# Performance work log

Hardware: AMD Instinct MI355X
Metric: run time of the kernel (lower is better)

Reference implementation:

```python
import jax, jax.numpy as jnp
import numpy as np

D_MODEL = 1024
N_HEAD = 16
HEAD_DIM = D_MODEL // N_HEAD


def setup_inputs() -> dict:
    key = jax.random.key(0)
    ks = jax.random.split(key, 8)
    B, T, C = 4, 2048, D_MODEL
    scale = 1.0 / np.sqrt(C)
    return {
        "q": jax.random.normal(ks[0], (B, T, C), dtype=jnp.float32),
        "k": jax.random.normal(ks[1], (B, T, C), dtype=jnp.float32),
        "v": jax.random.normal(ks[2], (B, T, C), dtype=jnp.float32),
        # torch.nn.Linear weights are (out_features, in_features)
        "Wq": jax.random.normal(ks[3], (C, C), dtype=jnp.float32) * scale,
        "Wk": jax.random.normal(ks[4], (C, C), dtype=jnp.float32) * scale,
        "Wv": jax.random.normal(ks[5], (C, C), dtype=jnp.float32) * scale,
        "Wo": jax.random.normal(ks[6], (C, C), dtype=jnp.float32) * scale,
        "bo": jax.random.normal(ks[7], (C,), dtype=jnp.float32) * scale,
    }


def reference(q, k, v, Wq, Wk, Wv, Wo, bo):
    B, T, C = q.shape
    # projections (torch Linear: x @ W.T), split into heads -> (B, H, T, Dh)
    def split_heads(x, W):
        y = jnp.einsum('btc,oc->bto', x, W)
        return y.reshape(B, T, N_HEAD, HEAD_DIM).transpose(0, 2, 1, 3)

    qh = split_heads(q, Wq)
    kh = split_heads(k, Wk)
    vh = split_heads(v, Wv)

    # scaled dot-product attention with full T x T scores (as in source)
    scores = jnp.einsum('bhqd,bhkd->bhqk', qh, kh) / jnp.sqrt(
        jnp.asarray(HEAD_DIM, dtype=qh.dtype))
    attn = jax.nn.softmax(scores, axis=-1)
    out = jnp.einsum('bhqk,bhkd->bhqd', attn, vh)

    out = out.transpose(0, 2, 1, 3).reshape(B, T, C)
    # output projection (with bias); dropout is identity in eval mode
    return jnp.einsum('btc,oc->bto', out, Wo) + bo
```

## Files before the change

kernel.cpp:

```cpp
#include <hip/hip_runtime.h>

#define TSEQ  2048
#define NB    4
#define CDIM  1024
#define NHEAD 16
#define DH    64
#define MROWS (NB*TSEQ)

using bf16x8 = __attribute__((ext_vector_type(8))) __bf16;
using f32x4  = __attribute__((ext_vector_type(4))) float;
using u16x8  = __attribute__((ext_vector_type(8))) unsigned short;

__device__ __forceinline__ unsigned short f2bf(float x) {
  unsigned u = __float_as_uint(x);
  u += 0x7fffu + ((u >> 16) & 1u);
  return (unsigned short)(u >> 16);
}

__device__ __forceinline__ unsigned pkp(float lo, float hi) {
  return __builtin_amdgcn_perm(__float_as_uint(hi), __float_as_uint(lo), 0x07060302u);
}

__device__ __forceinline__ float fexp2(float x) {
  float r;
  asm("v_exp_f32 %0, %1" : "=v"(r) : "v"(x));
  return r;
}

__device__ __forceinline__ void gload_lds16(const void* g, void* l) {
  __builtin_amdgcn_global_load_lds(
      (const __attribute__((address_space(1))) void*)g,
      (__attribute__((address_space(3))) void*)l,
      16, 0, 0);
}

__global__ void cast3_f32_bf16(const float* __restrict__ a, const float* __restrict__ b,
                               const float* __restrict__ c, unsigned short* __restrict__ out,
                               int n) {
  const float* src = (blockIdx.y == 0) ? a : (blockIdx.y == 1) ? b : c;
  int i = (blockIdx.x * 256 + threadIdx.x) * 8;
  if (i >= n) return;
  float4 x = *(const float4*)(src + i);
  float4 y = *(const float4*)(src + i + 4);
  u16x8 r;
  r[0] = f2bf(x.x); r[1] = f2bf(x.y); r[2] = f2bf(x.z); r[3] = f2bf(x.w);
  r[4] = f2bf(y.x); r[5] = f2bf(y.y); r[6] = f2bf(y.z); r[7] = f2bf(y.w);
  *(u16x8*)(out + (size_t)blockIdx.y * n + i) = r;
}

__global__ void cast4_f32_bf16(const float* __restrict__ a, const float* __restrict__ b,
                               const float* __restrict__ c, const float* __restrict__ d,
                               unsigned short* __restrict__ out, int n) {
  const float* src = (blockIdx.y == 0) ? a : (blockIdx.y == 1) ? b
                   : (blockIdx.y == 2) ? c : d;
  int i = (blockIdx.x * 256 + threadIdx.x) * 8;
  if (i >= n) return;
  float4 x = *(const float4*)(src + i);
  float4 y = *(const float4*)(src + i + 4);
  u16x8 r;
  r[0] = f2bf(x.x); r[1] = f2bf(x.y); r[2] = f2bf(x.z); r[3] = f2bf(x.w);
  r[4] = f2bf(y.x); r[5] = f2bf(y.y); r[6] = f2bf(y.z); r[7] = f2bf(y.w);
  *(u16x8*)(out + (size_t)blockIdx.y * n + i) = r;
}

template<int MODE>
__global__ __launch_bounds__(256)
void gemm_bt(const unsigned short* __restrict__ A,
             const unsigned short* __restrict__ Bw,
             void* __restrict__ Cout,
             const float* __restrict__ bias,
             float qscale)
{
  constexpr int K  = CDIM;
  constexpr int BK = 64;
  __shared__ __attribute__((aligned(16))) unsigned short As[128 * BK];
  __shared__ __attribute__((aligned(16))) unsigned short Bs[128 * BK];

  const int tid = threadIdx.x;
  const int l   = tid & 63, w = tid >> 6;
  const int l16 = l & 15,  lq = l >> 4;
  const int wm  = w >> 1,  wn = w & 1;

  const int pz = (MODE == 0) ? blockIdx.z : 0;
  A  += (size_t)pz * MROWS * CDIM;
  Bw += (size_t)pz * CDIM * CDIM;
  const float oscale = (MODE == 0 && pz == 0) ? qscale : 1.0f;

  const int nwg  = gridDim.x * gridDim.y;
  const int orig = blockIdx.y * gridDim.x + blockIdx.x;
  const int wg   = (orig & 7) * (nwg >> 3) + (orig >> 3);
  const int m0   = (wg / gridDim.x) * 128, n0 = (wg % gridDim.x) * 128;

  f32x4 acc[4][4] = {};

  int srow[4], scol[4];
#pragma unroll
  for (int i = 0; i < 4; ++i) {
    int r = (i * 256 + tid) >> 3;
    srow[i] = r;
    scol[i] = (((tid & 7) ^ (r & 7)) << 3);
  }

  for (int kt = 0; kt < K; kt += BK) {
#pragma unroll
    for (int i = 0; i < 4; ++i) {
      gload_lds16(A  + (size_t)(m0 + srow[i]) * K + kt + scol[i],
                  (char*)As + (i * 256 + w * 64) * 16);
      gload_lds16(Bw + (size_t)(n0 + srow[i]) * K + kt + scol[i],
                  (char*)Bs + (i * 256 + w * 64) * 16);
    }
    __syncthreads();

#pragma unroll
    for (int kk = 0; kk < 2; ++kk) {
      bf16x8 af[4], bfr[4];
#pragma unroll
      for (int mi = 0; mi < 4; ++mi) {
        int row = wm * 64 + mi * 16 + l16;
        af[mi] = *(const bf16x8*)&As[row * BK + (((kk * 4 + lq) ^ (row & 7)) << 3)];
      }
#pragma unroll
      for (int nj = 0; nj < 4; ++nj) {
        int row = wn * 64 + nj * 16 + l16;
        bfr[nj] = *(const bf16x8*)&Bs[row * BK + (((kk * 4 + lq) ^ (row & 7)) << 3)];
      }
#pragma unroll
      for (int mi = 0; mi < 4; ++mi)
#pragma unroll
        for (int nj = 0; nj < 4; ++nj)
          acc[mi][nj] = __builtin_amdgcn_mfma_f32_16x16x32_bf16(af[mi], bfr[nj], acc[mi][nj], 0, 0, 0);
    }
    __syncthreads();
  }

#pragma unroll
  for (int mi = 0; mi < 4; ++mi) {
#pragma unroll
    for (int nj = 0; nj < 4; ++nj) {
      int gn = n0 + wn * 64 + nj * 16 + l16;
#pragma unroll
      for (int r = 0; r < 4; ++r) {
        int gm = m0 + wm * 64 + mi * 16 + lq * 4 + r;
        float v = acc[mi][nj][r];
        if constexpr (MODE == 0) {
          int b = gm >> 11, t = gm & (TSEQ - 1);
          int h = gn >> 6,  d = gn & 63;
          ((unsigned short*)Cout)[(size_t)pz * MROWS * CDIM +
              ((((size_t)b * NHEAD + h) * TSEQ + t) << 6) + d] = f2bf(v * oscale);
        } else {
          ((float*)Cout)[(size_t)gm * CDIM + gn] = v + bias[gn];
        }
      }
    }
  }
}

__global__ __launch_bounds__(256, 3)
void attn_fwd(const unsigned short* __restrict__ Qh,
              const unsigned short* __restrict__ Kh,
              const unsigned short* __restrict__ Vh,
              unsigned short* __restrict__ O)
{
  __shared__ __attribute__((aligned(16))) unsigned short Ks[2][64 * DH];
  __shared__ __attribute__((aligned(16))) unsigned short Vt[2][DH * 64];

  const int tid = threadIdx.x;
  const int l   = tid & 63, w = tid >> 6;
  const int l16 = l & 15,  lq = l >> 4;

  const int orig    = blockIdx.y * gridDim.x + blockIdx.x;
  const int logical = (orig & 7) * 128 + (orig >> 3);
  const int bh  = logical >> 4;
  const int q0  = (logical & 15) * 128;
  const size_t base = (size_t)bh * TSEQ * DH;

  bf16x8 qfA0, qfA1, qfB0, qfB1;
  {
    const unsigned short* qp = Qh + base + (size_t)(q0 + w * 32 + l16) * DH + lq * 8;
    qfA0 = *(const bf16x8*)qp;
    qfA1 = *(const bf16x8*)(qp + 32);
    qfB0 = *(const bf16x8*)(qp + 16 * DH);
    qfB1 = *(const bf16x8*)(qp + 16 * DH + 32);
  }

  union { unsigned short u[8]; bf16x8 v; } onesu;
#pragma unroll
  for (int i = 0; i < 8; ++i) onesu.u[i] = 0x3F80;
  const bf16x8 ones = onesu.v;

  f32x4 oaccA[4] = {}, oaccB[4] = {};
  f32x4 laccA = {}, laccB = {};

  const int vc  = tid & 7;
  const int vu  = tid >> 3;
  const int kva = ((vu >> 4) << 5) | (vu & 15);
  const int vslot = ((vu >> 4) << 5) | (((vu >> 2) & 3) << 3) |
                    ((vu & 1) << 2) | (((vu >> 1) & 1) << 1);

  int vAddr[8];
#pragma unroll
  for (int j = 0; j < 8; ++j) {
    int d = vc * 8 + j;
    vAddr[j] = ((d << 7) + (vslot << 1)) ^ ((((d & 7) ^ (d >> 3)) & 7) << 4);
  }
  int kAddr[8];
#pragma unroll
  for (int nj = 0; nj < 4; ++nj) {
    int row = nj * 16 + l16;
    kAddr[nj * 2 + 0] = (row << 7) + ((lq       ^ (row & 7)) << 4);
    kAddr[nj * 2 + 1] = (row << 7) + (((4 + lq) ^ (row & 7)) << 4);
  }
  int pvAddr[8];
#pragma unroll
  for (int dj = 0; dj < 4; ++dj) {
    int d  = dj * 16 + l16;
    int cx = (((d & 7) ^ (d >> 3)) & 7) << 4;
    pvAddr[dj * 2 + 0] = (((d << 6) + (lq << 3)) << 1) ^ cx;
    pvAddr[dj * 2 + 1] = (((d << 6) + 32 + (lq << 3)) << 1) ^ cx;
  }

  constexpr int TILE_STRIDE = 64 * DH;
  const int krow = tid >> 3;
  const int kcol = ((tid & 7) ^ (krow & 7)) << 3;
  const unsigned short* kPtr = Kh + base + (size_t)krow * DH + kcol;
  const unsigned short* vPtr = Vh + base + (size_t)kva * DH + vc * 8;

  auto stageK = [&](int bb) {
    gload_lds16(kPtr,           (char*)Ks + bb * 8192 + (w * 64) * 16);
    gload_lds16(kPtr + 32 * DH, (char*)Ks + bb * 8192 + (256 + w * 64) * 16);
  };
  auto loadV = [&](u16x8& v0, u16x8& v1) {
    v0 = *(const u16x8*)vPtr;
    v1 = *(const u16x8*)(vPtr + 16 * DH);
  };
  auto writeV = [&](int bb, u16x8 v0, u16x8 v1) {
    union { u16x8 v; unsigned u[4]; } a, b;
    a.v = v0; b.v = v1;
    char* vb = (char*)Vt + bb * 8192;
#pragma unroll
    for (int r = 0; r < 4; ++r) {
      unsigned w0 = __builtin_amdgcn_perm(b.u[r], a.u[r], 0x05040100u);
      unsigned w1 = __builtin_amdgcn_perm(b.u[r], a.u[r], 0x07060302u);
      *(unsigned*)(vb + vAddr[2 * r])     = w0;
      *(unsigned*)(vb + vAddr[2 * r + 1]) = w1;
    }
  };

  {
    u16x8 v0, v1;
    loadV(v0, v1);
    stageK(0);
    writeV(0, v0, v1);
    kPtr += TILE_STRIDE;
    vPtr += TILE_STRIDE;
  }
  __syncthreads();

  constexpr int NT = TSEQ / 64;

  auto body = [&](int bb, bool PF) {
    u16x8 nv0, nv1;
    if (PF) {
      loadV(nv0, nv1);
      stageK(bb ^ 1);
      kPtr += TILE_STRIDE;
      vPtr += TILE_STRIDE;
    }

    f32x4 sA[4] = {}, sB[4] = {};
    __builtin_amdgcn_s_setprio(1);
#pragma unroll
    for (int nj = 0; nj < 4; ++nj) {
      bf16x8 kf0 = *(const bf16x8*)((const char*)Ks + bb * 8192 + kAddr[nj * 2 + 0]);
      bf16x8 kf1 = *(const bf16x8*)((const char*)Ks + bb * 8192 + kAddr[nj * 2 + 1]);
      sA[nj] = __builtin_amdgcn_mfma_f32_16x16x32_bf16(kf0, qfA0, sA[nj], 0, 0, 0);
      sA[nj] = __builtin_amdgcn_mfma_f32_16x16x32_bf16(kf1, qfA1, sA[nj], 0, 0, 0);
      sB[nj] = __builtin_amdgcn_mfma_f32_16x16x32_bf16(kf0, qfB0, sB[nj], 0, 0, 0);
      sB[nj] = __builtin_amdgcn_mfma_f32_16x16x32_bf16(kf1, qfB1, sB[nj], 0, 0, 0);
    }
    __builtin_amdgcn_s_setprio(0);

#pragma unroll
    for (int nj = 0; nj < 4; ++nj)
#pragma unroll
      for (int r = 0; r < 4; ++r) {
        sA[nj][r] = fexp2(sA[nj][r]);
        sB[nj][r] = fexp2(sB[nj][r]);
      }

    union { unsigned d[4]; bf16x8 v; } pA0, pA1, pB0, pB1;
    pA0.d[0] = pkp(sA[0][0], sA[1][0]); pA0.d[1] = pkp(sA[0][2], sA[1][2]);
    pA0.d[2] = pkp(sA[0][1], sA[1][1]); pA0.d[3] = pkp(sA[0][3], sA[1][3]);
    pA1.d[0] = pkp(sA[2][0], sA[3][0]); pA1.d[1] = pkp(sA[2][2], sA[3][2]);
    pA1.d[2] = pkp(sA[2][1], sA[3][1]); pA1.d[3] = pkp(sA[2][3], sA[3][3]);
    pB0.d[0] = pkp(sB[0][0], sB[1][0]); pB0.d[1] = pkp(sB[0][2], sB[1][2]);
    pB0.d[2] = pkp(sB[0][1], sB[1][1]); pB0.d[3] = pkp(sB[0][3], sB[1][3]);
    pB1.d[0] = pkp(sB[2][0], sB[3][0]); pB1.d[1] = pkp(sB[2][2], sB[3][2]);
    pB1.d[2] = pkp(sB[2][1], sB[3][1]); pB1.d[3] = pkp(sB[2][3], sB[3][3]);

    __builtin_amdgcn_s_setprio(1);
    laccA = __builtin_amdgcn_mfma_f32_16x16x32_bf16(pA0.v, ones, laccA, 0, 0, 0);
    laccA = __builtin_amdgcn_mfma_f32_16x16x32_bf16(pA1.v, ones, laccA, 0, 0, 0);
    laccB = __builtin_amdgcn_mfma_f32_16x16x32_bf16(pB0.v, ones, laccB, 0, 0, 0);
    laccB = __builtin_amdgcn_mfma_f32_16x16x32_bf16(pB1.v, ones, laccB, 0, 0, 0);
    __builtin_amdgcn_s_setprio(0);

    if (PF) writeV(bb ^ 1, nv0, nv1);

    __builtin_amdgcn_s_setprio(1);
#pragma unroll
    for (int dj = 0; dj < 4; ++dj) {
#pragma unroll
      for (int c = 0; c < 2; ++c) {
        bf16x8 vf = *(const bf16x8*)((const char*)Vt + bb * 8192 + pvAddr[dj * 2 + c]);
        oaccA[dj] = __builtin_amdgcn_mfma_f32_16x16x32_bf16(c ? pA1.v : pA0.v, vf, oaccA[dj], 0, 0, 0);
        oaccB[dj] = __builtin_amdgcn_mfma_f32_16x16x32_bf16(c ? pB1.v : pB0.v, vf, oaccB[dj], 0, 0, 0);
      }
    }
    __builtin_amdgcn_s_setprio(0);
    __syncthreads();
  };

  for (int tt = 0; tt < NT - 2; tt += 2) {
    body(0, true);
    body(1, true);
  }
  body(0, true);
  body(1, false);

  const int b = bh >> 4, h = bh & (NHEAD - 1);
#pragma unroll
  for (int r = 0; r < 4; ++r) {
    float invA = 1.f / laccA[r];
    float invB = 1.f / laccB[r];
    size_t obA = ((size_t)b * TSEQ + (q0 + w * 32 + lq * 4 + r)) * CDIM + h * DH;
    size_t obB = obA + (size_t)16 * CDIM;
#pragma unroll
    for (int dj = 0; dj < 4; ++dj) {
      O[obA + dj * 16 + l16] = f2bf(oaccA[dj][r] * invA);
      O[obB + dj * 16 + l16] = f2bf(oaccB[dj][r] * invB);
    }
  }
}

extern "C" void kernel_launch(void* const* d_in, const int* in_sizes, int n_in,
                              void* d_out, int out_size, void* d_ws, size_t ws_size,
                              hipStream_t stream) {
  const float* q  = (const float*)d_in[0];
  const float* k  = (const float*)d_in[1];
  const float* v  = (const float*)d_in[2];
  const float* Wq = (const float*)d_in[3];
  const float* Wk = (const float*)d_in[4];
  const float* Wv = (const float*)d_in[5];
  const float* Wo = (const float*)d_in[6];
  const float* bo = (const float*)d_in[7];

  char* ws = (char*)d_ws;
  const size_t SZ_ACT = (size_t)MROWS * CDIM * 2;
  const size_t SZ_W   = (size_t)CDIM * CDIM * 2;
  unsigned short* qb  = (unsigned short*)(ws);
  unsigned short* wqb = (unsigned short*)(ws + 3 * SZ_ACT);
  unsigned short* wob = (unsigned short*)(ws + 3 * SZ_ACT + 3 * SZ_W);
  unsigned short* Qh  = (unsigned short*)(ws + 3 * SZ_ACT + 4 * SZ_W);
  unsigned short* Kh  = (unsigned short*)(ws + 4 * SZ_ACT + 4 * SZ_W);
  unsigned short* Vh  = (unsigned short*)(ws + 5 * SZ_ACT + 4 * SZ_W);
  unsigned short* AttO = qb;

  const int nAct = MROWS * CDIM;
  const int nW   = CDIM * CDIM;

  cast3_f32_bf16<<<dim3(nAct / 2048, 3), 256, 0, stream>>>(q, k, v, qb, nAct);
  cast4_f32_bf16<<<dim3(nW / 2048, 4), 256, 0, stream>>>(Wq, Wk, Wv, Wo, wqb, nW);

  const float QSCALE = 0.18033688011112042f;

  gemm_bt<0><<<dim3(CDIM / 128, MROWS / 128, 3), 256, 0, stream>>>(
      qb, wqb, Qh, nullptr, QSCALE);

  attn_fwd<<<dim3(TSEQ / 128, NB * NHEAD), 256, 0, stream>>>(Qh, Kh, Vh, AttO);

  gemm_bt<1><<<dim3(CDIM / 128, MROWS / 128, 1), 256, 0, stream>>>(
      AttO, wob, (float*)d_out, bo, 1.0f);
}
```

Before: 192.6 us.

## Software-pipeline attention: overlap PV of previous tile with QK of current tile

Restructures the attention inner loop so each iteration computes QK^T and softmax exp for tile i while running the P·V MFMAs for tile i-1 in the same high-priority block. This needs a triple-buffered V tile in LDS and ping-pong P registers, with a prologue and epilogue for the first and last tiles. LDS address arrays are replaced by computed offsets to save registers. The aim is to hide exp/pack latency behind matrix work, at the cost of extra LDS and live registers, which may reduce occupancy.

```diff
diff --git a/kernel.cpp b/kernel.cpp
--- a/kernel.cpp
+++ b/kernel.cpp
@@ -33,6 +33,8 @@
       (__attribute__((address_space(3))) void*)l,
       16, 0, 0);
 }
+
+#define MFMA16(a, b, c) __builtin_amdgcn_mfma_f32_16x16x32_bf16((a), (b), (c), 0, 0, 0)
 
 __global__ void cast3_f32_bf16(const float* __restrict__ a, const float* __restrict__ b,
                                const float* __restrict__ c, unsigned short* __restrict__ out,
@@ -128,7 +130,7 @@
       for (int mi = 0; mi < 4; ++mi)
 #pragma unroll
         for (int nj = 0; nj < 4; ++nj)
-          acc[mi][nj] = __builtin_amdgcn_mfma_f32_16x16x32_bf16(af[mi], bfr[nj], acc[mi][nj], 0, 0, 0);
+          acc[mi][nj] = MFMA16(af[mi], bfr[nj], acc[mi][nj]);
     }
     __syncthreads();
   }
@@ -162,7 +164,7 @@
               unsigned short* __restrict__ O)
 {
   __shared__ __attribute__((aligned(16))) unsigned short Ks[2][64 * DH];
-  __shared__ __attribute__((aligned(16))) unsigned short Vt[2][DH * 64];
+  __shared__ __attribute__((aligned(16))) unsigned short Vt[3][DH * 64];
 
   const int tid = threadIdx.x;
   const int l   = tid & 63, w = tid >> 6;
@@ -196,20 +198,11 @@
   const int kva = ((vu >> 4) << 5) | (vu & 15);
   const int vslot = ((vu >> 4) << 5) | (((vu >> 2) & 3) << 3) |
                     ((vu & 1) << 2) | (((vu >> 1) & 1) << 1);
-
-  int vAddr[8];
-#pragma unroll
-  for (int j = 0; j < 8; ++j) {
-    int d = vc * 8 + j;
-    vAddr[j] = ((d << 7) + (vslot << 1)) ^ ((((d & 7) ^ (d >> 3)) & 7) << 4);
-  }
-  int kAddr[8];
-#pragma unroll
-  for (int nj = 0; nj < 4; ++nj) {
-    int row = nj * 16 + l16;
-    kAddr[nj * 2 + 0] = (row << 7) + ((lq       ^ (row & 7)) << 4);
-    kAddr[nj * 2 + 1] = (row << 7) + (((4 + lq) ^ (row & 7)) << 4);
-  }
+  const int vvx = (vc << 10) | ((vslot << 1) ^ (vc << 4));
+
+  const int kB0 = (l16 << 7) + ((lq ^ (l16 & 7)) << 4);
+  const int kB1 = (l16 << 7) + (((4 + lq) ^ (l16 & 7)) << 4);
+
   int pvAddr[8];
 #pragma unroll
   for (int dj = 0; dj < 4; ++dj) {
@@ -225,61 +218,56 @@
   const unsigned short* kPtr = Kh + base + (size_t)krow * DH + kcol;
   const unsigned short* vPtr = Vh + base + (size_t)kva * DH + vc * 8;
 
-  auto stageK = [&](int bb) {
-    gload_lds16(kPtr,           (char*)Ks + bb * 8192 + (w * 64) * 16);
-    gload_lds16(kPtr + 32 * DH, (char*)Ks + bb * 8192 + (256 + w * 64) * 16);
+  auto stageK = [&](int kb) {
+    gload_lds16(kPtr,           (char*)Ks + kb * 8192 + (w * 64) * 16);
+    gload_lds16(kPtr + 32 * DH, (char*)Ks + kb * 8192 + (256 + w * 64) * 16);
   };
   auto loadV = [&](u16x8& v0, u16x8& v1) {
     v0 = *(const u16x8*)vPtr;
     v1 = *(const u16x8*)(vPtr + 16 * DH);
   };
-  auto writeV = [&](int bb, u16x8 v0, u16x8 v1) {
+  auto writeV = [&](int vb_i, u16x8 v0, u16x8 v1) {
     union { u16x8 v; unsigned u[4]; } a, b;
     a.v = v0; b.v = v1;
-    char* vb = (char*)Vt + bb * 8192;
+    char* vb = (char*)Vt + vb_i * 8192;
 #pragma unroll
     for (int r = 0; r < 4; ++r) {
       unsigned w0 = __builtin_amdgcn_perm(b.u[r], a.u[r], 0x05040100u);
       unsigned w1 = __builtin_amdgcn_perm(b.u[r], a.u[r], 0x07060302u);
-      *(unsigned*)(vb + vAddr[2 * r])     = w0;
-      *(unsigned*)(vb + vAddr[2 * r + 1]) = w1;
+      int j0 = 2 * r, j1 = 2 * r + 1;
+      *(unsigned*)(vb + ((vvx ^ (j0 << 4)) + j0 * 128)) = w0;
+      *(unsigned*)(vb + ((vvx ^ (j1 << 4)) + j1 * 128)) = w1;
     }
   };
+
+  bf16x8 peA0, peA1, peB0, peB1, poA0, poA1, poB0, poB1;
 
   {
     u16x8 v0, v1;
     loadV(v0, v1);
     stageK(0);
     writeV(0, v0, v1);
-    kPtr += TILE_STRIDE;
-    vPtr += TILE_STRIDE;
+    kPtr += TILE_STRIDE; vPtr += TILE_STRIDE;
   }
   __syncthreads();
 
-  constexpr int NT = TSEQ / 64;
-
-  auto body = [&](int bb, bool PF) {
+  {
     u16x8 nv0, nv1;
-    if (PF) {
-      loadV(nv0, nv1);
-      stageK(bb ^ 1);
-      kPtr += TILE_STRIDE;
-      vPtr += TILE_STRIDE;
-    }
-
+    loadV(nv0, nv1);
+    stageK(1);
+    kPtr += TILE_STRIDE; vPtr += TILE_STRIDE;
+
+    const char* ksC = (const char*)Ks;
     f32x4 sA[4] = {}, sB[4] = {};
     __builtin_amdgcn_s_setprio(1);
 #pragma unroll
     for (int nj = 0; nj < 4; ++nj) {
-      bf16x8 kf0 = *(const bf16x8*)((const char*)Ks + bb * 8192 + kAddr[nj * 2 + 0]);
-      bf16x8 kf1 = *(const bf16x8*)((const char*)Ks + bb * 8192 + kAddr[nj * 2 + 1]);
-      sA[nj] = __builtin_amdgcn_mfma_f32_16x16x32_bf16(kf0, qfA0, sA[nj], 0, 0, 0);
-      sA[nj] = __builtin_amdgcn_mfma_f32_16x16x32_bf16(kf1, qfA1, sA[nj], 0, 0, 0);
-      sB[nj] = __builtin_amdgcn_mfma_f32_16x16x32_bf16(kf0, qfB0, sB[nj], 0, 0, 0);
-      sB[nj] = __builtin_amdgcn_mfma_f32_16x16x32_bf16(kf1, qfB1, sB[nj], 0, 0, 0);
+      bf16x8 kf0 = *(const bf16x8*)(ksC + nj * 2048 + kB0);
+      bf16x8 kf1 = *(const bf16x8*)(ksC + nj * 2048 + kB1);
+      sA[nj] = MFMA16(kf0, qfA0, sA[nj]); sA[nj] = MFMA16(kf1, qfA1, sA[nj]);
+      sB[nj] = MFMA16(kf0, qfB0, sB[nj]); sB[nj] = MFMA16(kf1, qfB1, sB[nj]);
     }
     __builtin_amdgcn_s_setprio(0);
-
 #pragma unroll
     for (int nj = 0; nj < 4; ++nj)
 #pragma unroll
@@ -287,46 +275,94 @@
         sA[nj][r] = fexp2(sA[nj][r]);
         sB[nj][r] = fexp2(sB[nj][r]);
       }
-
-    union { unsigned d[4]; bf16x8 v; } pA0, pA1, pB0, pB1;
-    pA0.d[0] = pkp(sA[0][0], sA[1][0]); pA0.d[1] = pkp(sA[0][2], sA[1][2]);
-    pA0.d[2] = pkp(sA[0][1], sA[1][1]); pA0.d[3] = pkp(sA[0][3], sA[1][3]);
-    pA1.d[0] = pkp(sA[2][0], sA[3][0]); pA1.d[1] = pkp(sA[2][2], sA[3][2]);
-    pA1.d[2] = pkp(sA[2][1], sA[3][1]); pA1.d[3] = pkp(sA[2][3], sA[3][3]);
-    pB0.d[0] = pkp(sB[0][0], sB[1][0]); pB0.d[1] = pkp(sB[0][2], sB[1][2]);
-    pB0.d[2] = pkp(sB[0][1], sB[1][1]); pB0.d[3] = pkp(sB[0][3], sB[1][3]);
-    pB1.d[0] = pkp(sB[2][0], sB[3][0]); pB1.d[1] = pkp(sB[2][2], sB[3][2]);
-    pB1.d[2] = pkp(sB[2][1], sB[3][1]); pB1.d[3] = pkp(sB[2][3], sB[3][3]);
-
+    union { unsigned d[4]; bf16x8 v; } uA0, uA1, uB0, uB1;
+    uA0.d[0] = pkp(sA[0][0], sA[1][0]); uA0.d[1] = pkp(sA[0][2], sA[1][2]);
+    uA0.d[2] = pkp(sA[0][1], sA[1][1]); uA0.d[3] = pkp(sA[0][3], sA[1][3]);
+    uA1.d[0] = pkp(sA[2][0], sA[3][0]); uA1.d[1] = pkp(sA[2][2], sA[3][2]);
+    uA1.d[2] = pkp(sA[2][1], sA[3][1]); uA1.d[3] = pkp(sA[2][3], sA[3][3]);
+    uB0.d[0] = pkp(sB[0][0], sB[1][0]); uB0.d[1] = pkp(sB[0][2], sB[1][2]);
+    uB0.d[2] = pkp(sB[0][1], sB[1][1]); uB0.d[3] = pkp(sB[0][3], sB[1][3]);
+    uB1.d[0] = pkp(sB[2][0], sB[3][0]); uB1.d[1] = pkp(sB[2][2], sB[3][2]);
+    uB1.d[2] = pkp(sB[2][1], sB[3][1]); uB1.d[3] = pkp(sB[2][3], sB[3][3]);
+    peA0 = uA0.v; peA1 = uA1.v; peB0 = uB0.v; peB1 = uB1.v;
+    laccA = MFMA16(peA0, ones, laccA); laccA = MFMA16(peA1, ones, laccA);
+    laccB = MFMA16(peB0, ones, laccB); laccB = MFMA16(peB1, ones, laccB);
+    writeV(1, nv0, nv1);
+    __syncthreads();
+  }
+
+  auto body = [&](int kb, int vr, int vw, bool pf,
+                  const bf16x8& rA0, const bf16x8& rA1, const bf16x8& rB0, const bf16x8& rB1,
+                  bf16x8& wA0, bf16x8& wA1, bf16x8& wB0, bf16x8& wB1) {
+    u16x8 nv0, nv1;
+    if (pf) {
+      loadV(nv0, nv1);
+      stageK(kb ^ 1);
+      kPtr += TILE_STRIDE; vPtr += TILE_STRIDE;
+    }
+    const char* ksC = (const char*)Ks + kb * 8192;
+    const char* vtC = (const char*)Vt + vr * 8192;
+
+    f32x4 sA[4] = {}, sB[4] = {};
     __builtin_amdgcn_s_setprio(1);
-    laccA = __builtin_amdgcn_mfma_f32_16x16x32_bf16(pA0.v, ones, laccA, 0, 0, 0);
-    laccA = __builtin_amdgcn_mfma_f32_16x16x32_bf16(pA1.v, ones, laccA, 0, 0, 0);
-    laccB = __builtin_amdgcn_mfma_f32_16x16x32_bf16(pB0.v, ones, laccB, 0, 0, 0);
-    laccB = __builtin_amdgcn_mfma_f32_16x16x32_bf16(pB1.v, ones, laccB, 0, 0, 0);
+#pragma unroll
+    for (int nj = 0; nj < 4; ++nj) {
+      bf16x8 kf0 = *(const bf16x8*)(ksC + nj * 2048 + kB0);
+      bf16x8 kf1 = *(const bf16x8*)(ksC + nj * 2048 + kB1);
+      sA[nj] = MFMA16(kf0, qfA0, sA[nj]); sA[nj] = MFMA16(kf1, qfA1, sA[nj]);
+      sB[nj] = MFMA16(kf0, qfB0, sB[nj]); sB[nj] = MFMA16(kf1, qfB1, sB[nj]);
+    }
+#pragma unroll
+    for (int dj = 0; dj < 4; ++dj) {
+      bf16x8 vf0 = *(const bf16x8*)(vtC + pvAddr[dj * 2 + 0]);
+      bf16x8 vf1 = *(const bf16x8*)(vtC + pvAddr[dj * 2 + 1]);
+      oaccA[dj] = MFMA16(rA0, vf0, oaccA[dj]); oaccA[dj] = MFMA16(rA1, vf1, oaccA[dj]);
+      oaccB[dj] = MFMA16(rB0, vf0, oaccB[dj]); oaccB[dj] = MFMA16(rB1, vf1, oaccB[dj]);
+    }
     __builtin_amdgcn_s_setprio(0);
-
-    if (PF) writeV(bb ^ 1, nv0, nv1);
-
-    __builtin_amdgcn_s_setprio(1);
-#pragma unroll
-    for (int dj = 0; dj < 4; ++dj) {
-#pragma unroll
-      for (int c = 0; c < 2; ++c) {
-        bf16x8 vf = *(const bf16x8*)((const char*)Vt + bb * 8192 + pvAddr[dj * 2 + c]);
-        oaccA[dj] = __builtin_amdgcn_mfma_f32_16x16x32_bf16(c ? pA1.v : pA0.v, vf, oaccA[dj], 0, 0, 0);
-        oaccB[dj] = __builtin_amdgcn_mfma_f32_16x16x32_bf16(c ? pB1.v : pB0.v, vf, oaccB[dj], 0, 0, 0);
+#pragma unroll
+    for (int nj = 0; nj < 4; ++nj)
+#pragma unroll
+      for (int r = 0; r < 4; ++r) {
+        sA[nj][r] = fexp2(sA[nj][r]);
+        sB[nj][r] = fexp2(sB[nj][r]);
       }
-    }
-    __builtin_amdgcn_s_setprio(0);
+    union { unsigned d[4]; bf16x8 v; } uA0, uA1, uB0, uB1;
+    uA0.d[0] = pkp(sA[0][0], sA[1][0]); uA0.d[1] = pkp(sA[0][2], sA[1][2]);
+    uA0.d[2] = pkp(sA[0][1], sA[1][1]); uA0.d[3] = pkp(sA[0][3], sA[1][3]);
+    uA1.d[0] = pkp(sA[2][0], sA[3][0]); uA1.d[1] = pkp(sA[2][2], sA[3][2]);
+    uA1.d[2] = pkp(sA[2][1], sA[3][1]); uA1.d[3] = pkp(sA[2][3], sA[3][3]);
+    uB0.d[0] = pkp(sB[0][0], sB[1][0]); uB0.d[1] = pkp(sB[0][2], sB[1][2]);
+    uB0.d[2] = pkp(sB[0][1], sB[1][1]); uB0.d[3] = pkp(sB[0][3], sB[1][3]);
+    uB1.d[0] = pkp(sB[2][0], sB[3][0]); uB1.d[1] = pkp(sB[2][2], sB[3][2]);
+    uB1.d[2] = pkp(sB[2][1], sB[3][1]); uB1.d[3] = pkp(sB[2][3], sB[3][3]);
+    wA0 = uA0.v; wA1 = uA1.v; wB0 = uB0.v; wB1 = uB1.v;
+    laccA = MFMA16(wA0, ones, laccA); laccA = MFMA16(wA1, ones, laccA);
+    laccB = MFMA16(wB0, ones, laccB); laccB = MFMA16(wB1, ones, laccB);
+    if (pf) writeV(vw, nv0, nv1);
     __syncthreads();
   };
 
-  for (int tt = 0; tt < NT - 2; tt += 2) {
-    body(0, true);
-    body(1, true);
-  }
-  body(0, true);
-  body(1, false);
+  for (int i = 0; i < 5; ++i) {
+    body(1, 0, 2, true, peA0, peA1, peB0, peB1, poA0, poA1, poB0, poB1);
+    body(0, 1, 0, true, poA0, poA1, poB0, poB1, peA0, peA1, peB0, peB1);
+    body(1, 2, 1, true, peA0, peA1, peB0, peB1, poA0, poA1, poB0, poB1);
+    body(0, 0, 2, true, poA0, poA1, poB0, poB1, peA0, peA1, peB0, peB1);
+    body(1, 1, 0, true, peA0, peA1, peB0, peB1, poA0, poA1, poB0, poB1);
+    body(0, 2, 1, true, poA0, poA1, poB0, poB1, peA0, peA1, peB0, peB1);
+  }
+  body(1, 0, 0, false, peA0, peA1, peB0, peB1, poA0, poA1, poB0, poB1);
+
+  {
+    const char* vtC = (const char*)Vt + 1 * 8192;
+#pragma unroll
+    for (int dj = 0; dj < 4; ++dj) {
+      bf16x8 vf0 = *(const bf16x8*)(vtC + pvAddr[dj * 2 + 0]);
+      bf16x8 vf1 = *(const bf16x8*)(vtC + pvAddr[dj * 2 + 1]);
+      oaccA[dj] = MFMA16(poA0, vf0, oaccA[dj]); oaccA[dj] = MFMA16(poA1, vf1, oaccA[dj]);
+      oaccB[dj] = MFMA16(poB0, vf0, oaccB[dj]); oaccB[dj] = MFMA16(poB1, vf1, oaccB[dj]);
+    }
+  }
 
   const int b = bh >> 4, h = bh & (NHEAD - 1);
 #pragma unroll
```

Measured after the change: 191.9 us. About the same (-0.4%).
